# Kernel optimization log

Measured on AMD Instinct MI355X. Metric: run time of the kernel, lower is better.

The kernel has to match this reference:

```python
import jax, jax.numpy as jnp
import numpy as np

B, N, C = 8, 4096, 64          # graphs, points per graph, feature dim
RATIO = 0.25
M = int(N * RATIO)             # 1024 sampled centroids per graph
R = 0.2                        # radius (points live in the unit cube)
K = 64                         # max_num_neighbors in the forward
BIG = 1e10


def fps_single(pos):
    """Farthest point sampling on one cloud. pos: [N,3] -> [M] local indices.
    Deterministic start at index 0 (PyG uses a random start; math is identical)."""
    n = pos.shape[0]

    def step(carry, _):
        mind, last = carry
        d = jnp.sum((pos - pos[last]) ** 2, axis=-1)      # [N]
        mind = jnp.minimum(mind, d)
        nxt = jnp.argmax(mind)
        return (mind, nxt), nxt

    init = (jnp.full((n,), BIG, pos.dtype), jnp.int32(0))
    _, rest = jax.lax.scan(step, init, None, length=M - 1)
    return jnp.concatenate([jnp.zeros((1,), rest.dtype), rest])


def setup_inputs() -> dict:
    key = jax.random.key(0)
    ks = jax.random.split(key, 8)
    x = jax.random.normal(ks[0], (B * N, C), dtype=jnp.float32)
    pos = jax.random.uniform(ks[1], (B * N, 3), dtype=jnp.float32)
    batch = jnp.repeat(jnp.arange(B, dtype=jnp.int64), N)
    seed_idx = jnp.arange(B * N, dtype=jnp.int64)
    d_in, h, f_out = C + 3, 128, 256
    W1 = jax.random.normal(ks[2], (d_in, h), dtype=jnp.float32) / np.sqrt(d_in)
    b1 = jnp.zeros((h,), jnp.float32)
    W2 = jax.random.normal(ks[3], (h, h), dtype=jnp.float32) / np.sqrt(h)
    b2 = jnp.zeros((h,), jnp.float32)
    W3 = jax.random.normal(ks[4], (h, f_out), dtype=jnp.float32) / np.sqrt(h)
    b3 = jnp.zeros((f_out,), jnp.float32)
    return {"x": x, "pos": pos, "batch": batch, "seed_idx": seed_idx,
            "W1": W1, "b1": b1, "W2": W2, "b2": b2, "W3": W3, "b3": b3}


def reference(x, pos, batch, seed_idx, W1, b1, W2, b2, W3, b3):
    posb = pos.reshape(B, N, 3)
    xb = x.reshape(B, N, C)

    # --- FPS per graph (batch is block-contiguous with N points per graph) ---
    idx_local = jax.vmap(fps_single)(posb)                     # [B, M]
    ctr = jax.vmap(lambda p, i: p[i])(posb, idx_local)         # [B, M, 3]

    # --- radius neighbor search: up to K neighbors within r of each centroid ---
    d2 = jnp.sum((ctr[:, :, None, :] - posb[:, None, :, :]) ** 2, axis=-1)  # [B,M,N]
    d2m = jnp.where(d2 < R * R, d2, BIG)
    neg_d, nbr = jax.lax.top_k(-d2m, K)                        # K nearest within r
    valid = (-neg_d) < R * R                                   # [B, M, K]

    # --- PointConv: msg = MLP([x_j, pos_j - pos_i]), max-aggregate ---
    x_j = jax.vmap(lambda a, i: a[i])(xb, nbr)                 # [B, M, K, C]
    pos_j = jax.vmap(lambda p, i: p[i])(posb, nbr)             # [B, M, K, 3]
    msg = jnp.concatenate([x_j, pos_j - ctr[:, :, None, :]], axis=-1)  # [B,M,K,C+3]
    h = jax.nn.relu(msg @ W1 + b1)
    h = jax.nn.relu(h @ W2 + b2)
    h = jax.nn.relu(h @ W3 + b3)                               # [B, M, K, 256]
    h = jnp.where(valid[..., None], h, -BIG)
    out = jnp.max(h, axis=2)                                   # [B, M, 256]
    out = jnp.where(jnp.any(valid, axis=-1)[..., None], out, 0.0)

    # --- gather sampled outputs back to the flat layout ---
    idx_flat = (idx_local + jnp.arange(B)[:, None] * N).reshape(-1)  # [B*M]
    x_out = out.reshape(B * M, -1)
    pos_out = pos[idx_flat]
    batch_out = batch[idx_flat]
    seed_out = seed_idx[idx_flat]
    return x_out, pos_out, batch_out, seed_out
```

## Files before the change

### kernel.cpp

```cpp
#include <hip/hip_runtime.h>
#include <stdint.h>

#define BB 8
#define NN 4096
#define CC 64
#define MM 1024
#define EE (BB*MM)
#define KK 64
#define F3 256
#define SM 104
#define SH 136
#define CAP 768

typedef __bf16 bf16x8 __attribute__((ext_vector_type(8)));
typedef float floatx4 __attribute__((ext_vector_type(4)));

#define DPP_MAXSTEP(ctrl, rmask) { \
    unsigned o = (unsigned)__builtin_amdgcn_update_dpp(0, (int)v, ctrl, rmask, 0xf, false); \
    v = v > o ? v : o; }
__device__ __forceinline__ unsigned wave_umax_u32(unsigned v) {
  DPP_MAXSTEP(0x111, 0xf)
  DPP_MAXSTEP(0x112, 0xf)
  DPP_MAXSTEP(0x114, 0xf)
  DPP_MAXSTEP(0x118, 0xf)
  DPP_MAXSTEP(0x142, 0xa)
  DPP_MAXSTEP(0x143, 0xc)
  return (unsigned)__builtin_amdgcn_readlane((int)v, 63);
}
#define DPP_MINSTEP(ctrl, rmask) { \
    unsigned o = (unsigned)__builtin_amdgcn_update_dpp((int)0xffffffffu, (int)v, ctrl, rmask, 0xf, false); \
    v = v < o ? v : o; }
__device__ __forceinline__ unsigned wave_umin_u32(unsigned v) {
  DPP_MINSTEP(0x111, 0xf)
  DPP_MINSTEP(0x112, 0xf)
  DPP_MINSTEP(0x114, 0xf)
  DPP_MINSTEP(0x118, 0xf)
  DPP_MINSTEP(0x142, 0xa)
  DPP_MINSTEP(0x143, 0xc)
  return (unsigned)__builtin_amdgcn_readlane((int)v, 63);
}

__global__ __launch_bounds__(512) void fps_prep_kernel(
    const float* __restrict__ pos,
    const float* __restrict__ W1, const float* __restrict__ W2, const float* __restrict__ W3,
    int* __restrict__ fpsIdx, float* __restrict__ ctr,
    __bf16* __restrict__ W1t, __bf16* __restrict__ W2t, __bf16* __restrict__ W3t,
    float4* __restrict__ pos4) {
  __shared__ float4 sP4[NN];
  __shared__ unsigned long long sRed[2][8];
  const int blk = blockIdx.x;
  const int t = threadIdx.x;

  if (blk >= BB) {
    if (blk < 128) {
      const int i0 = (blk - 8) * 512 + t;
      if (i0 < 128 * 96) {
        const int n = i0 / 96, k = i0 % 96;
        W1t[i0] = (k < 67) ? (__bf16)W1[k * 128 + n] : (__bf16)0.0f;
      } else if (i0 < 128 * 96 + 128 * 128) {
        const int i = i0 - 128 * 96;
        const int n = i / 128, k = i % 128;
        W2t[i] = (__bf16)W2[k * 128 + n];
      } else {
        const int i = i0 - (128 * 96 + 128 * 128);
        const int n = i / 128, k = i % 128;
        W3t[i] = (__bf16)W3[k * 256 + n];
      }
    } else {
      const int i = (blk - 128) * 512 + t;
      pos4[i] = make_float4(pos[(long)i * 3 + 0], pos[(long)i * 3 + 1],
                            pos[(long)i * 3 + 2], 0.0f);
    }
    return;
  }

  const int g = blk;
  const int lane = t & 63, wv = t >> 6;
  float px[8], py[8], pz[8], mind[8];
#pragma unroll
  for (int j = 0; j < 8; ++j) {
    const int p = t + (j << 9);
    const long base = ((long)g * NN + p) * 3;
    px[j] = pos[base + 0];
    py[j] = pos[base + 1];
    pz[j] = pos[base + 2];
    mind[j] = 1e10f;
    sP4[p] = make_float4(px[j], py[j], pz[j], 0.0f);
  }
  __syncthreads();
  float wx = sP4[0].x, wy = sP4[0].y, wz = sP4[0].z;
  int win0 = 0, win1 = 0;
  for (int s = 1; s < MM; ++s) {
    unsigned bb = 0u, bidx = (unsigned)t;
#pragma unroll
    for (int j = 0; j < 8; ++j) {
      const float dx = __fsub_rn(px[j], wx);
      const float dy = __fsub_rn(py[j], wy);
      const float dz = __fsub_rn(pz[j], wz);
      const float d2 = __fadd_rn(__fadd_rn(__fmul_rn(dx, dx), __fmul_rn(dy, dy)), __fmul_rn(dz, dz));
      mind[j] = fminf(mind[j], d2);
      const unsigned mb = __float_as_uint(mind[j]);
      if (mb > bb) { bb = mb; bidx = (unsigned)(t + (j << 9)); }
    }
    const unsigned maxv = wave_umax_u32(bb);
    const unsigned cand = (bb == maxv) ? bidx : 0xffffffffu;
    const unsigned minidx = wave_umin_u32(cand);
    if (lane == 0)
      sRed[s & 1][wv] = ((unsigned long long)maxv << 32) | (unsigned long long)(~minidx);
    __syncthreads();
    unsigned long long m = sRed[s & 1][0];
#pragma unroll
    for (int w = 1; w < 8; ++w) {
      const unsigned long long o = sRed[s & 1][w];
      m = o > m ? o : m;
    }
    const int widx = (int)(~(unsigned)m);
    const float4 wp = sP4[widx];
    wx = wp.x; wy = wp.y; wz = wp.z;
    if (s == t)       win0 = widx;
    if (s == t + 512) win1 = widx;
  }
  {
    const long e0 = (long)g * MM + t;
    const float4 p0 = sP4[win0];
    fpsIdx[e0] = win0;
    ctr[e0 * 3 + 0] = p0.x; ctr[e0 * 3 + 1] = p0.y; ctr[e0 * 3 + 2] = p0.z;
    const long e1 = e0 + 512;
    const float4 p1 = sP4[win1];
    fpsIdx[e1] = win1;
    ctr[e1 * 3 + 0] = p1.x; ctr[e1 * 3 + 1] = p1.y; ctr[e1 * 3 + 2] = p1.z;
  }
}

__global__ __launch_bounds__(512) void mlp_kernel(const float* __restrict__ x,
    const float4* __restrict__ pos4, const float* __restrict__ ctr,
    const int* __restrict__ fpsIdx,
    const __bf16* __restrict__ W1t, const __bf16* __restrict__ W2t,
    const __bf16* __restrict__ W3t,
    const float* __restrict__ b1, const float* __restrict__ b2,
    const float* __restrict__ b3,
    float* __restrict__ outX, float* __restrict__ outP,
    float* __restrict__ outB, float* __restrict__ outS) {
  __shared__ __align__(16) __bf16 sMsg[64 * SM];
  __shared__ __align__(16) __bf16 sH[64 * SH];
  __shared__ int sSel[KK];
  __shared__ int sCnt;
  unsigned long long* sDI = (unsigned long long*)sMsg;

  const int e = blockIdx.x;
  const int t = threadIdx.x;
  const int b = e >> 10;
  const int lane = t & 63, wv = t >> 6;

  if (t == 0) sCnt = 0;
  const float cx = ctr[(long)e * 3 + 0];
  const float cy = ctr[(long)e * 3 + 1];
  const float cz = ctr[(long)e * 3 + 2];
  if (t < 3) outP[(long)e * 3 + t] = ctr[(long)e * 3 + t];
  if (t == 3) { outB[e] = (float)b; outS[e] = (float)(b * NN + fpsIdx[e]); }
  const float R2 = (float)(0.2 * 0.2);
  __syncthreads();

#pragma unroll
  for (int q = 0; q < NN / 512; ++q) {
    const int p = t + q * 512;
    const float4 P = pos4[b * NN + p];
    const float dx = __fsub_rn(cx, P.x);
    const float dy = __fsub_rn(cy, P.y);
    const float dz = __fsub_rn(cz, P.z);
    const float d2 = __fadd_rn(__fadd_rn(__fmul_rn(dx, dx), __fmul_rn(dy, dy)), __fmul_rn(dz, dz));
    const bool v = d2 < R2;
    const unsigned long long mask = __ballot(v);
    int wbase = 0;
    if (lane == 0 && mask) wbase = atomicAdd(&sCnt, (int)__popcll(mask));
    wbase = __shfl(wbase, 0);
    if (v) {
      const int off = wbase + (int)__popcll(mask & ((1ull << lane) - 1ull));
      if (off < CAP)
        sDI[off] = ((unsigned long long)__float_as_uint(d2) << 32) | (unsigned)p;
    }
  }
  __syncthreads();
  int cnt = sCnt; cnt = cnt > CAP ? CAP : cnt;
  const int nsel = cnt < KK ? cnt : KK;

  for (int i = t; i < cnt; i += 512) {
    const unsigned long long my = sDI[i];
    int rank = 0;
#pragma unroll 8
    for (int j = 0; j < cnt; ++j) rank += (sDI[j] < my) ? 1 : 0;
    if (rank < KK) sSel[rank] = (int)(unsigned)(my & 0xffffffffu);
  }
  __syncthreads();
  cnt = nsel;

  {
    const int r = t >> 3, p = t & 7;
    float4 a = make_float4(0.f, 0.f, 0.f, 0.f), c4 = a;
    if (r < cnt) {
      const float* xr = x + (long)(b * NN + sSel[r]) * CC + p * 8;
      a  = *(const float4*)xr;
      c4 = *(const float4*)(xr + 4);
    }
    __bf16 o[8] = {(__bf16)a.x, (__bf16)a.y, (__bf16)a.z, (__bf16)a.w,
                   (__bf16)c4.x, (__bf16)c4.y, (__bf16)c4.z, (__bf16)c4.w};
    *(uint4*)&sMsg[r * SM + p * 8] = *(uint4*)o;
  }
  if (t < 64) {
    const int r = t;
    __bf16 d0 = (__bf16)0.0f, d1 = (__bf16)0.0f, d2v = (__bf16)0.0f;
    if (r < cnt) {
      const float4 P = pos4[b * NN + sSel[r]];
      d0  = (__bf16)__fsub_rn(P.x, cx);
      d1  = (__bf16)__fsub_rn(P.y, cy);
      d2v = (__bf16)__fsub_rn(P.z, cz);
    }
    sMsg[r * SM + 64] = d0;
    sMsg[r * SM + 65] = d1;
    sMsg[r * SM + 66] = d2v;
    for (int c = 67; c < SM; ++c) sMsg[r * SM + c] = (__bf16)0.0f;
  }
  __syncthreads();

  const int l15 = lane & 15, quad = lane >> 4;
  {
    floatx4 acc[4] = {};
    const __bf16* wrow = W1t + (wv * 16 + l15) * 96;
#pragma unroll
    for (int ks = 0; ks < 3; ++ks) {
      const bf16x8 bfrag = *(const bf16x8*)(wrow + ks * 32 + quad * 8);
#pragma unroll
      for (int mt = 0; mt < 4; ++mt) {
        const bf16x8 afrag = *(const bf16x8*)&sMsg[(mt * 16 + l15) * SM + ks * 32 + quad * 8];
        acc[mt] = __builtin_amdgcn_mfma_f32_16x16x32_bf16(afrag, bfrag, acc[mt], 0, 0, 0);
      }
    }
    const int col = wv * 16 + l15;
    const float bias = b1[col];
#pragma unroll
    for (int mt = 0; mt < 4; ++mt)
#pragma unroll
      for (int rg = 0; rg < 4; ++rg) {
        const int row = mt * 16 + quad * 4 + rg;
        float v = acc[mt][rg] + bias;
        v = v > 0.0f ? v : 0.0f;
        sH[row * SH + col] = (__bf16)v;
      }
  }
  __syncthreads();
  {
    floatx4 acc[4] = {};
    const __bf16* wrow = W2t + (wv * 16 + l15) * 128;
#pragma unroll
    for (int ks = 0; ks < 4; ++ks) {
      const bf16x8 bfrag = *(const bf16x8*)(wrow + ks * 32 + quad * 8);
#pragma unroll
      for (int mt = 0; mt < 4; ++mt) {
        const bf16x8 afrag = *(const bf16x8*)&sH[(mt * 16 + l15) * SH + ks * 32 + quad * 8];
        acc[mt] = __builtin_amdgcn_mfma_f32_16x16x32_bf16(afrag, bfrag, acc[mt], 0, 0, 0);
      }
    }
    __syncthreads();
    const int col = wv * 16 + l15;
    const float bias = b2[col];
#pragma unroll
    for (int mt = 0; mt < 4; ++mt)
#pragma unroll
      for (int rg = 0; rg < 4; ++rg) {
        const int row = mt * 16 + quad * 4 + rg;
        float v = acc[mt][rg] + bias;
        v = v > 0.0f ? v : 0.0f;
        sH[row * SH + col] = (__bf16)v;
      }
  }
  __syncthreads();
  {
    floatx4 acc[2][4] = {};
#pragma unroll
    for (int ks = 0; ks < 4; ++ks) {
      bf16x8 afrag[4];
#pragma unroll
      for (int mt = 0; mt < 4; ++mt)
        afrag[mt] = *(const bf16x8*)&sH[(mt * 16 + l15) * SH + ks * 32 + quad * 8];
#pragma unroll
      for (int i = 0; i < 2; ++i) {
        const bf16x8 bfrag = *(const bf16x8*)(W3t + ((wv * 2 + i) * 16 + l15) * 128 + ks * 32 + quad * 8);
#pragma unroll
        for (int mt = 0; mt < 4; ++mt)
          acc[i][mt] = __builtin_amdgcn_mfma_f32_16x16x32_bf16(afrag[mt], bfrag, acc[i][mt], 0, 0, 0);
      }
    }
#pragma unroll
    for (int i = 0; i < 2; ++i) {
      const int col = (wv * 2 + i) * 16 + l15;
      const float bias = b3[col];
      float mx = 0.0f;
#pragma unroll
      for (int mt = 0; mt < 4; ++mt)
#pragma unroll
        for (int rg = 0; rg < 4; ++rg) {
          const int row = mt * 16 + quad * 4 + rg;
          float v = acc[i][mt][rg] + bias;
          v = v > 0.0f ? v : 0.0f;
          if (row < cnt) mx = fmaxf(mx, v);
        }
      mx = fmaxf(mx, __shfl_xor(mx, 16));
      mx = fmaxf(mx, __shfl_xor(mx, 32));
      if (quad == 0) outX[(long)e * F3 + col] = mx;
    }
  }
}

extern "C" void kernel_launch(void* const* d_in, const int* in_sizes, int n_in,
                              void* d_out, int out_size, void* d_ws, size_t ws_size,
                              hipStream_t stream) {
  const float* x   = (const float*)d_in[0];
  const float* pos = (const float*)d_in[1];
  const float* W1  = (const float*)d_in[4];
  const float* b1  = (const float*)d_in[5];
  const float* W2  = (const float*)d_in[6];
  const float* b2  = (const float*)d_in[7];
  const float* W3  = (const float*)d_in[8];
  const float* b3  = (const float*)d_in[9];

  char* ws = (char*)d_ws;
  int*    fpsIdx = (int*)(ws);
  float*  ctr    = (float*)(ws + 32768);
  __bf16* W1t    = (__bf16*)(ws + 131072);
  __bf16* W2t    = (__bf16*)(ws + 155648);
  __bf16* W3t    = (__bf16*)(ws + 188416);
  float4* pos4   = (float4*)(ws + 253952);

  float* outX = (float*)d_out;
  float* outP = outX + (long)EE * F3;
  float* outB = outP + (long)EE * 3;
  float* outS = outB + EE;

  fps_prep_kernel<<<192, 512, 0, stream>>>(pos, W1, W2, W3,
                                           fpsIdx, ctr, W1t, W2t, W3t, pos4);
  mlp_kernel<<<EE, 512, 0, stream>>>(x, pos4, ctr, fpsIdx, W1t, W2t, W3t,
                                     b1, b2, b3, outX, outP, outB, outS);
}
```

Measured before the change: 859.6 us.

## Fuse FPS, weight prep and MLP into one persistent kernel with progress flags

Merges the FPS/prep kernel and the per-centroid MLP kernel into a single launch. Blocks take work in order through an atomic ticket: FPS groups come first, then weight-transpose blocks, then centroid blocks. Each FPS group publishes its centroids in chunks of 64 through release flags, so MLP blocks can start once their centroid is ready instead of waiting for all FPS work to finish. The FPS loop also switches to packed f32 math and broadcasts the winner's coordinates by readlane rather than an LDS lookup, and the pos4 repack is dropped in favour of direct strided pos reads. This trades a kernel boundary for spin-waiting, and it depends on the FPS blocks staying resident and making forward progress.

```diff
diff --git a/kernel.cpp b/kernel.cpp
--- a/kernel.cpp
+++ b/kernel.cpp
@@ -11,9 +11,11 @@
 #define SM 104
 #define SH 136
 #define CAP 768
+#define NPREP 120
 
 typedef __bf16 bf16x8 __attribute__((ext_vector_type(8)));
 typedef float floatx4 __attribute__((ext_vector_type(4)));
+typedef float floatx2 __attribute__((ext_vector_type(2)));
 
 #define DPP_MAXSTEP(ctrl, rmask) { \
     unsigned o = (unsigned)__builtin_amdgcn_update_dpp(0, (int)v, ctrl, rmask, 0xf, false); \
@@ -40,134 +42,182 @@
   return (unsigned)__builtin_amdgcn_readlane((int)v, 63);
 }
 
-__global__ __launch_bounds__(512) void fps_prep_kernel(
-    const float* __restrict__ pos,
-    const float* __restrict__ W1, const float* __restrict__ W2, const float* __restrict__ W3,
+__global__ __launch_bounds__(512, 6) void fused_kernel(
+    const float* __restrict__ x, const float* __restrict__ pos,
+    const float* __restrict__ W1, const float* __restrict__ b1,
+    const float* __restrict__ W2, const float* __restrict__ b2,
+    const float* __restrict__ W3, const float* __restrict__ b3,
+    unsigned* __restrict__ flags,
     int* __restrict__ fpsIdx, float* __restrict__ ctr,
     __bf16* __restrict__ W1t, __bf16* __restrict__ W2t, __bf16* __restrict__ W3t,
-    float4* __restrict__ pos4) {
-  __shared__ float4 sP4[NN];
-  __shared__ unsigned long long sRed[2][8];
-  const int blk = blockIdx.x;
-  const int t = threadIdx.x;
-
-  if (blk >= BB) {
-    if (blk < 128) {
-      const int i0 = (blk - 8) * 512 + t;
-      if (i0 < 128 * 96) {
-        const int n = i0 / 96, k = i0 % 96;
-        W1t[i0] = (k < 67) ? (__bf16)W1[k * 128 + n] : (__bf16)0.0f;
-      } else if (i0 < 128 * 96 + 128 * 128) {
-        const int i = i0 - 128 * 96;
-        const int n = i / 128, k = i % 128;
-        W2t[i] = (__bf16)W2[k * 128 + n];
-      } else {
-        const int i = i0 - (128 * 96 + 128 * 128);
-        const int n = i / 128, k = i % 128;
-        W3t[i] = (__bf16)W3[k * 256 + n];
-      }
-    } else {
-      const int i = (blk - 128) * 512 + t;
-      pos4[i] = make_float4(pos[(long)i * 3 + 0], pos[(long)i * 3 + 1],
-                            pos[(long)i * 3 + 2], 0.0f);
-    }
-    return;
-  }
-
-  const int g = blk;
-  const int lane = t & 63, wv = t >> 6;
-  float px[8], py[8], pz[8], mind[8];
-#pragma unroll
-  for (int j = 0; j < 8; ++j) {
-    const int p = t + (j << 9);
-    const long base = ((long)g * NN + p) * 3;
-    px[j] = pos[base + 0];
-    py[j] = pos[base + 1];
-    pz[j] = pos[base + 2];
-    mind[j] = 1e10f;
-    sP4[p] = make_float4(px[j], py[j], pz[j], 0.0f);
-  }
-  __syncthreads();
-  float wx = sP4[0].x, wy = sP4[0].y, wz = sP4[0].z;
-  int win0 = 0, win1 = 0;
-  for (int s = 1; s < MM; ++s) {
-    unsigned bb = 0u, bidx = (unsigned)t;
-#pragma unroll
-    for (int j = 0; j < 8; ++j) {
-      const float dx = __fsub_rn(px[j], wx);
-      const float dy = __fsub_rn(py[j], wy);
-      const float dz = __fsub_rn(pz[j], wz);
-      const float d2 = __fadd_rn(__fadd_rn(__fmul_rn(dx, dx), __fmul_rn(dy, dy)), __fmul_rn(dz, dz));
-      mind[j] = fminf(mind[j], d2);
-      const unsigned mb = __float_as_uint(mind[j]);
-      if (mb > bb) { bb = mb; bidx = (unsigned)(t + (j << 9)); }
-    }
-    const unsigned maxv = wave_umax_u32(bb);
-    const unsigned cand = (bb == maxv) ? bidx : 0xffffffffu;
-    const unsigned minidx = wave_umin_u32(cand);
-    if (lane == 0)
-      sRed[s & 1][wv] = ((unsigned long long)maxv << 32) | (unsigned long long)(~minidx);
-    __syncthreads();
-    unsigned long long m = sRed[s & 1][0];
-#pragma unroll
-    for (int w = 1; w < 8; ++w) {
-      const unsigned long long o = sRed[s & 1][w];
-      m = o > m ? o : m;
-    }
-    const int widx = (int)(~(unsigned)m);
-    const float4 wp = sP4[widx];
-    wx = wp.x; wy = wp.y; wz = wp.z;
-    if (s == t)       win0 = widx;
-    if (s == t + 512) win1 = widx;
-  }
-  {
-    const long e0 = (long)g * MM + t;
-    const float4 p0 = sP4[win0];
-    fpsIdx[e0] = win0;
-    ctr[e0 * 3 + 0] = p0.x; ctr[e0 * 3 + 1] = p0.y; ctr[e0 * 3 + 2] = p0.z;
-    const long e1 = e0 + 512;
-    const float4 p1 = sP4[win1];
-    fpsIdx[e1] = win1;
-    ctr[e1 * 3 + 0] = p1.x; ctr[e1 * 3 + 1] = p1.y; ctr[e1 * 3 + 2] = p1.z;
-  }
-}
-
-__global__ __launch_bounds__(512) void mlp_kernel(const float* __restrict__ x,
-    const float4* __restrict__ pos4, const float* __restrict__ ctr,
-    const int* __restrict__ fpsIdx,
-    const __bf16* __restrict__ W1t, const __bf16* __restrict__ W2t,
-    const __bf16* __restrict__ W3t,
-    const float* __restrict__ b1, const float* __restrict__ b2,
-    const float* __restrict__ b3,
     float* __restrict__ outX, float* __restrict__ outP,
     float* __restrict__ outB, float* __restrict__ outS) {
   __shared__ __align__(16) __bf16 sMsg[64 * SM];
   __shared__ __align__(16) __bf16 sH[64 * SH];
   __shared__ int sSel[KK];
   __shared__ int sCnt;
+  __shared__ unsigned long long sRedK[2][8];
+  __shared__ __align__(16) float4 sRedP[2][8];
+  __shared__ int sTicket;
+
+  const int t = threadIdx.x;
+  const int lane = t & 63, wv = t >> 6;
+  if (t == 0)
+    sTicket = (int)__hip_atomic_fetch_add(&flags[0], 1u, __ATOMIC_RELAXED,
+                                          __HIP_MEMORY_SCOPE_AGENT);
+  __syncthreads();
+  const int tk = sTicket;
+
+  if (tk < BB) {
+    __builtin_amdgcn_s_setprio(3);
+    const int g = tk;
+    floatx2 p2x[4], p2y[4], p2z[4];
+    float mind[8];
+#pragma unroll
+    for (int q = 0; q < 4; ++q) {
+#pragma unroll
+      for (int h = 0; h < 2; ++h) {
+        const int p = t + (((q << 1) | h) << 9);
+        const long base = ((long)g * NN + p) * 3;
+        p2x[q][h] = pos[base + 0];
+        p2y[q][h] = pos[base + 1];
+        p2z[q][h] = pos[base + 2];
+        mind[(q << 1) | h] = 1e10f;
+      }
+    }
+    float wx = pos[(long)g * NN * 3 + 0];
+    float wy = pos[(long)g * NN * 3 + 1];
+    float wz = pos[(long)g * NN * 3 + 2];
+    int winI0 = 0, winI1 = 0;
+    float w0x = wx, w0y = wy, w0z = wz;
+    float w1x = wx, w1y = wy, w1z = wz;
+
+    for (int s = 1; s < MM; ++s) {
+      const float nwx = -wx, nwy = -wy, nwz = -wz;
+      const floatx2 nx2 = {nwx, nwx}, ny2 = {nwy, nwy}, nz2 = {nwz, nwz};
+      unsigned bb = 0u, bidx = (unsigned)t;
+#pragma unroll
+      for (int q = 0; q < 4; ++q) {
+        floatx2 dx, dy, dz, xx, yy, zz, s1, d2;
+        asm("v_pk_add_f32 %0, %1, %2" : "=v"(dx) : "v"(p2x[q]), "v"(nx2));
+        asm("v_pk_add_f32 %0, %1, %2" : "=v"(dy) : "v"(p2y[q]), "v"(ny2));
+        asm("v_pk_add_f32 %0, %1, %2" : "=v"(dz) : "v"(p2z[q]), "v"(nz2));
+        asm("v_pk_mul_f32 %0, %1, %1" : "=v"(xx) : "v"(dx));
+        asm("v_pk_mul_f32 %0, %1, %1" : "=v"(yy) : "v"(dy));
+        asm("v_pk_mul_f32 %0, %1, %1" : "=v"(zz) : "v"(dz));
+        asm("v_pk_add_f32 %0, %1, %2" : "=v"(s1) : "v"(xx), "v"(yy));
+        asm("v_pk_add_f32 %0, %1, %2" : "=v"(d2) : "v"(s1), "v"(zz));
+#pragma unroll
+        for (int h = 0; h < 2; ++h) {
+          const int i = (q << 1) | h;
+          mind[i] = fminf(mind[i], d2[h]);
+          const unsigned mb = __float_as_uint(mind[i]);
+          if (mb > bb) { bb = mb; bidx = (unsigned)(t + (i << 9)); }
+        }
+      }
+      const unsigned maxv = wave_umax_u32(bb);
+      const unsigned cand = (bb == maxv) ? bidx : 0xffffffffu;
+      const unsigned minidx = wave_umin_u32(cand);
+      const int jw = (int)(minidx >> 9), qw = jw >> 1, hw = jw & 1;
+      const floatx2 sx = p2x[qw], sy = p2y[qw], sz = p2z[qw];
+      const float cxx = hw ? sx[1] : sx[0];
+      const float cyy = hw ? sy[1] : sy[0];
+      const float czz = hw ? sz[1] : sz[0];
+      const int lw = (int)(minidx & 63u);
+      const float bx = __int_as_float(__builtin_amdgcn_readlane(__float_as_int(cxx), lw));
+      const float by = __int_as_float(__builtin_amdgcn_readlane(__float_as_int(cyy), lw));
+      const float bz = __int_as_float(__builtin_amdgcn_readlane(__float_as_int(czz), lw));
+      if (lane == 0) {
+        sRedK[s & 1][wv] = ((unsigned long long)maxv << 32) |
+                           (unsigned long long)(~minidx);
+        sRedP[s & 1][wv] = make_float4(bx, by, bz, 0.0f);
+      }
+      __syncthreads();
+      unsigned long long kk = sRedK[s & 1][0];
+      int wbest = 0;
+#pragma unroll
+      for (int w = 1; w < 8; ++w) {
+        const unsigned long long kw = sRedK[s & 1][w];
+        if (kw > kk) { kk = kw; wbest = w; }
+      }
+      const float4 wp = sRedP[s & 1][wbest];
+      wx = wp.x; wy = wp.y; wz = wp.z;
+      const int widx = (int)(~(unsigned)kk);
+      if (s == t)       { winI0 = widx; w0x = wx; w0y = wy; w0z = wz; }
+      if (s == t + 512) { winI1 = widx; w1x = wx; w1y = wy; w1z = wz; }
+      if ((s & 63) == 63) {
+        const int f = s >> 6;
+        if (wv == (f & 7)) {
+          const int step = (f < 8) ? t : (t + 512);
+          const int wI   = (f < 8) ? winI0 : winI1;
+          const float fx = (f < 8) ? w0x : w1x;
+          const float fy = (f < 8) ? w0y : w1y;
+          const float fz = (f < 8) ? w0z : w1z;
+          const long ee = (long)g * MM + step;
+          __hip_atomic_store(&fpsIdx[ee], wI, __ATOMIC_RELAXED, __HIP_MEMORY_SCOPE_AGENT);
+          __hip_atomic_store(&ctr[ee * 3 + 0], fx, __ATOMIC_RELAXED, __HIP_MEMORY_SCOPE_AGENT);
+          __hip_atomic_store(&ctr[ee * 3 + 1], fy, __ATOMIC_RELAXED, __HIP_MEMORY_SCOPE_AGENT);
+          __hip_atomic_store(&ctr[ee * 3 + 2], fz, __ATOMIC_RELAXED, __HIP_MEMORY_SCOPE_AGENT);
+          if (lane == 0)
+            __hip_atomic_store(&flags[2 + g], (unsigned)((f + 1) * 64),
+                               __ATOMIC_RELEASE, __HIP_MEMORY_SCOPE_AGENT);
+        }
+      }
+    }
+    return;
+  }
+
+  if (tk < BB + NPREP) {
+    const int i0 = (tk - BB) * 512 + t;
+    if (i0 < 128 * 96) {
+      const int n = i0 / 96, k = i0 % 96;
+      W1t[i0] = (k < 67) ? (__bf16)W1[k * 128 + n] : (__bf16)0.0f;
+    } else if (i0 < 128 * 96 + 128 * 128) {
+      const int i = i0 - 128 * 96;
+      const int n = i / 128, k = i % 128;
+      W2t[i] = (__bf16)W2[k * 128 + n];
+    } else {
+      const int i = i0 - (128 * 96 + 128 * 128);
+      const int n = i / 128, k = i % 128;
+      W3t[i] = (__bf16)W3[k * 256 + n];
+    }
+    __syncthreads();
+    if (t == 0)
+      __hip_atomic_fetch_add(&flags[1], 1u, __ATOMIC_RELEASE, __HIP_MEMORY_SCOPE_AGENT);
+    return;
+  }
+
+  const int eo = tk - (BB + NPREP);
+  const int b = eo & 7;
+  const int m = eo >> 3;
+  const int e = b * MM + m;
+
+  if (t == 1) sCnt = 0;
+  if (t == 0) {
+    while (__hip_atomic_load(&flags[1], __ATOMIC_RELAXED, __HIP_MEMORY_SCOPE_AGENT) < NPREP)
+      __builtin_amdgcn_s_sleep(32);
+    while ((int)__hip_atomic_load(&flags[2 + b], __ATOMIC_RELAXED, __HIP_MEMORY_SCOPE_AGENT) <= m)
+      __builtin_amdgcn_s_sleep(32);
+    (void)__hip_atomic_load(&flags[1], __ATOMIC_ACQUIRE, __HIP_MEMORY_SCOPE_AGENT);
+    (void)__hip_atomic_load(&flags[2 + b], __ATOMIC_ACQUIRE, __HIP_MEMORY_SCOPE_AGENT);
+  }
+  __syncthreads();
+
   unsigned long long* sDI = (unsigned long long*)sMsg;
-
-  const int e = blockIdx.x;
-  const int t = threadIdx.x;
-  const int b = e >> 10;
-  const int lane = t & 63, wv = t >> 6;
-
-  if (t == 0) sCnt = 0;
   const float cx = ctr[(long)e * 3 + 0];
   const float cy = ctr[(long)e * 3 + 1];
   const float cz = ctr[(long)e * 3 + 2];
   if (t < 3) outP[(long)e * 3 + t] = ctr[(long)e * 3 + t];
   if (t == 3) { outB[e] = (float)b; outS[e] = (float)(b * NN + fpsIdx[e]); }
   const float R2 = (float)(0.2 * 0.2);
-  __syncthreads();
+  const long pbase = (long)b * NN * 3;
 
 #pragma unroll
   for (int q = 0; q < NN / 512; ++q) {
     const int p = t + q * 512;
-    const float4 P = pos4[b * NN + p];
-    const float dx = __fsub_rn(cx, P.x);
-    const float dy = __fsub_rn(cy, P.y);
-    const float dz = __fsub_rn(cz, P.z);
+    const float dx = __fsub_rn(cx, pos[pbase + (long)p * 3 + 0]);
+    const float dy = __fsub_rn(cy, pos[pbase + (long)p * 3 + 1]);
+    const float dz = __fsub_rn(cz, pos[pbase + (long)p * 3 + 2]);
     const float d2 = __fadd_rn(__fadd_rn(__fmul_rn(dx, dx), __fmul_rn(dy, dy)), __fmul_rn(dz, dz));
     const bool v = d2 < R2;
     const unsigned long long mask = __ballot(v);
@@ -204,16 +254,17 @@
     }
     __bf16 o[8] = {(__bf16)a.x, (__bf16)a.y, (__bf16)a.z, (__bf16)a.w,
                    (__bf16)c4.x, (__bf16)c4.y, (__bf16)c4.z, (__bf16)c4.w};
+    __syncthreads();
     *(uint4*)&sMsg[r * SM + p * 8] = *(uint4*)o;
   }
   if (t < 64) {
     const int r = t;
     __bf16 d0 = (__bf16)0.0f, d1 = (__bf16)0.0f, d2v = (__bf16)0.0f;
     if (r < cnt) {
-      const float4 P = pos4[b * NN + sSel[r]];
-      d0  = (__bf16)__fsub_rn(P.x, cx);
-      d1  = (__bf16)__fsub_rn(P.y, cy);
-      d2v = (__bf16)__fsub_rn(P.z, cz);
+      const long j = pbase + (long)sSel[r] * 3;
+      d0  = (__bf16)__fsub_rn(pos[j + 0], cx);
+      d1  = (__bf16)__fsub_rn(pos[j + 1], cy);
+      d2v = (__bf16)__fsub_rn(pos[j + 2], cz);
     }
     sMsg[r * SM + 64] = d0;
     sMsg[r * SM + 65] = d1;
@@ -324,20 +375,20 @@
   const float* b3  = (const float*)d_in[9];
 
   char* ws = (char*)d_ws;
-  int*    fpsIdx = (int*)(ws);
-  float*  ctr    = (float*)(ws + 32768);
-  __bf16* W1t    = (__bf16*)(ws + 131072);
-  __bf16* W2t    = (__bf16*)(ws + 155648);
-  __bf16* W3t    = (__bf16*)(ws + 188416);
-  float4* pos4   = (float4*)(ws + 253952);
+  unsigned* flags  = (unsigned*)(ws);
+  int*    fpsIdx = (int*)(ws + 1024);
+  float*  ctr    = (float*)(ws + 33792);
+  __bf16* W1t    = (__bf16*)(ws + 132096);
+  __bf16* W2t    = (__bf16*)(ws + 156672);
+  __bf16* W3t    = (__bf16*)(ws + 189440);
 
   float* outX = (float*)d_out;
   float* outP = outX + (long)EE * F3;
   float* outB = outP + (long)EE * 3;
   float* outS = outB + EE;
 
-  fps_prep_kernel<<<192, 512, 0, stream>>>(pos, W1, W2, W3,
-                                           fpsIdx, ctr, W1t, W2t, W3t, pos4);
-  mlp_kernel<<<EE, 512, 0, stream>>>(x, pos4, ctr, fpsIdx, W1t, W2t, W3t,
-                                     b1, b2, b3, outX, outP, outB, outS);
+  hipMemsetAsync(flags, 0, 64, stream);
+  fused_kernel<<<BB + NPREP + EE, 512, 0, stream>>>(
+      x, pos, W1, b1, W2, b2, W3, b3,
+      flags, fpsIdx, ctr, W1t, W2t, W3t, outX, outP, outB, outS);
 }
```

New measurement: 1.724 ms. 101% more time.

## Pass FPS winner coordinates through per-wave reduction and use packed f32 math

Applied to the files above, without the earlier changes.

The FPS loop no longer keeps the whole point cloud in shared memory. Each wave reads its candidate winner's coordinates from registers with readlane and publishes them beside the reduction key, so the serial loop no longer does a dependent shared-memory lookup of the winning point after the barrier. The distance computation uses v_pk_add/v_pk_mul f32 inline asm to handle two points per instruction, with the subtraction rewritten as adding a negated value, which should round the same way. A __syncthreads was also added in the MLP kernel before the sMsg write, which looks like a fix for a hazard where sMsg is reused from sDI.

```diff
diff --git a/kernel.cpp b/kernel.cpp
--- a/kernel.cpp
+++ b/kernel.cpp
@@ -14,6 +14,7 @@
 
 typedef __bf16 bf16x8 __attribute__((ext_vector_type(8)));
 typedef float floatx4 __attribute__((ext_vector_type(4)));
+typedef float floatx2 __attribute__((ext_vector_type(2)));
 
 #define DPP_MAXSTEP(ctrl, rmask) { \
     unsigned o = (unsigned)__builtin_amdgcn_update_dpp(0, (int)v, ctrl, rmask, 0xf, false); \
@@ -46,8 +47,8 @@
     int* __restrict__ fpsIdx, float* __restrict__ ctr,
     __bf16* __restrict__ W1t, __bf16* __restrict__ W2t, __bf16* __restrict__ W3t,
     float4* __restrict__ pos4) {
-  __shared__ float4 sP4[NN];
-  __shared__ unsigned long long sRed[2][8];
+  __shared__ unsigned long long sRedK[2][8];
+  __shared__ __align__(16) float4 sRedP[2][8];
   const int blk = blockIdx.x;
   const int t = threadIdx.x;
 
@@ -76,59 +77,88 @@
 
   const int g = blk;
   const int lane = t & 63, wv = t >> 6;
-  float px[8], py[8], pz[8], mind[8];
-#pragma unroll
-  for (int j = 0; j < 8; ++j) {
-    const int p = t + (j << 9);
-    const long base = ((long)g * NN + p) * 3;
-    px[j] = pos[base + 0];
-    py[j] = pos[base + 1];
-    pz[j] = pos[base + 2];
-    mind[j] = 1e10f;
-    sP4[p] = make_float4(px[j], py[j], pz[j], 0.0f);
-  }
-  __syncthreads();
-  float wx = sP4[0].x, wy = sP4[0].y, wz = sP4[0].z;
-  int win0 = 0, win1 = 0;
+  floatx2 p2x[4], p2y[4], p2z[4];
+  float mind[8];
+#pragma unroll
+  for (int q = 0; q < 4; ++q) {
+#pragma unroll
+    for (int h = 0; h < 2; ++h) {
+      const int p = t + (((q << 1) | h) << 9);
+      const long base = ((long)g * NN + p) * 3;
+      p2x[q][h] = pos[base + 0];
+      p2y[q][h] = pos[base + 1];
+      p2z[q][h] = pos[base + 2];
+      mind[(q << 1) | h] = 1e10f;
+    }
+  }
+  float wx = pos[(long)g * NN * 3 + 0];
+  float wy = pos[(long)g * NN * 3 + 1];
+  float wz = pos[(long)g * NN * 3 + 2];
+  int winI0 = 0, winI1 = 0;
+  float w0x = wx, w0y = wy, w0z = wz;
+  float w1x = wx, w1y = wy, w1z = wz;
+
   for (int s = 1; s < MM; ++s) {
+    const float nwx = -wx, nwy = -wy, nwz = -wz;
+    const floatx2 nx2 = {nwx, nwx}, ny2 = {nwy, nwy}, nz2 = {nwz, nwz};
     unsigned bb = 0u, bidx = (unsigned)t;
 #pragma unroll
-    for (int j = 0; j < 8; ++j) {
-      const float dx = __fsub_rn(px[j], wx);
-      const float dy = __fsub_rn(py[j], wy);
-      const float dz = __fsub_rn(pz[j], wz);
-      const float d2 = __fadd_rn(__fadd_rn(__fmul_rn(dx, dx), __fmul_rn(dy, dy)), __fmul_rn(dz, dz));
-      mind[j] = fminf(mind[j], d2);
-      const unsigned mb = __float_as_uint(mind[j]);
-      if (mb > bb) { bb = mb; bidx = (unsigned)(t + (j << 9)); }
+    for (int q = 0; q < 4; ++q) {
+      floatx2 dx, dy, dz, xx, yy, zz, s1, d2;
+      asm("v_pk_add_f32 %0, %1, %2" : "=v"(dx) : "v"(p2x[q]), "v"(nx2));
+      asm("v_pk_add_f32 %0, %1, %2" : "=v"(dy) : "v"(p2y[q]), "v"(ny2));
+      asm("v_pk_add_f32 %0, %1, %2" : "=v"(dz) : "v"(p2z[q]), "v"(nz2));
+      asm("v_pk_mul_f32 %0, %1, %1" : "=v"(xx) : "v"(dx));
+      asm("v_pk_mul_f32 %0, %1, %1" : "=v"(yy) : "v"(dy));
+      asm("v_pk_mul_f32 %0, %1, %1" : "=v"(zz) : "v"(dz));
+      asm("v_pk_add_f32 %0, %1, %2" : "=v"(s1) : "v"(xx), "v"(yy));
+      asm("v_pk_add_f32 %0, %1, %2" : "=v"(d2) : "v"(s1), "v"(zz));
+#pragma unroll
+      for (int h = 0; h < 2; ++h) {
+        const int i = (q << 1) | h;
+        mind[i] = fminf(mind[i], d2[h]);
+        const unsigned mb = __float_as_uint(mind[i]);
+        if (mb > bb) { bb = mb; bidx = (unsigned)(t + (i << 9)); }
+      }
     }
     const unsigned maxv = wave_umax_u32(bb);
     const unsigned cand = (bb == maxv) ? bidx : 0xffffffffu;
     const unsigned minidx = wave_umin_u32(cand);
-    if (lane == 0)
-      sRed[s & 1][wv] = ((unsigned long long)maxv << 32) | (unsigned long long)(~minidx);
+    const int jw = (int)(minidx >> 9), qw = jw >> 1, hw = jw & 1;
+    const floatx2 sx = p2x[qw], sy = p2y[qw], sz = p2z[qw];
+    const float cxx = hw ? sx[1] : sx[0];
+    const float cyy = hw ? sy[1] : sy[0];
+    const float czz = hw ? sz[1] : sz[0];
+    const int lw = (int)(minidx & 63u);
+    const float bx = __int_as_float(__builtin_amdgcn_readlane(__float_as_int(cxx), lw));
+    const float by = __int_as_float(__builtin_amdgcn_readlane(__float_as_int(cyy), lw));
+    const float bz = __int_as_float(__builtin_amdgcn_readlane(__float_as_int(czz), lw));
+    if (lane == 0) {
+      sRedK[s & 1][wv] = ((unsigned long long)maxv << 32) |
+                         (unsigned long long)(~minidx);
+      sRedP[s & 1][wv] = make_float4(bx, by, bz, 0.0f);
+    }
     __syncthreads();
-    unsigned long long m = sRed[s & 1][0];
+    unsigned long long kk = sRedK[s & 1][0];
+    int wbest = 0;
 #pragma unroll
     for (int w = 1; w < 8; ++w) {
-      const unsigned long long o = sRed[s & 1][w];
-      m = o > m ? o : m;
-    }
-    const int widx = (int)(~(unsigned)m);
-    const float4 wp = sP4[widx];
+      const unsigned long long kw = sRedK[s & 1][w];
+      if (kw > kk) { kk = kw; wbest = w; }
+    }
+    const float4 wp = sRedP[s & 1][wbest];
     wx = wp.x; wy = wp.y; wz = wp.z;
-    if (s == t)       win0 = widx;
-    if (s == t + 512) win1 = widx;
+    const int widx = (int)(~(unsigned)kk);
+    if (s == t)       { winI0 = widx; w0x = wx; w0y = wy; w0z = wz; }
+    if (s == t + 512) { winI1 = widx; w1x = wx; w1y = wy; w1z = wz; }
   }
   {
     const long e0 = (long)g * MM + t;
-    const float4 p0 = sP4[win0];
-    fpsIdx[e0] = win0;
-    ctr[e0 * 3 + 0] = p0.x; ctr[e0 * 3 + 1] = p0.y; ctr[e0 * 3 + 2] = p0.z;
+    fpsIdx[e0] = winI0;
+    ctr[e0 * 3 + 0] = w0x; ctr[e0 * 3 + 1] = w0y; ctr[e0 * 3 + 2] = w0z;
     const long e1 = e0 + 512;
-    const float4 p1 = sP4[win1];
-    fpsIdx[e1] = win1;
-    ctr[e1 * 3 + 0] = p1.x; ctr[e1 * 3 + 1] = p1.y; ctr[e1 * 3 + 2] = p1.z;
+    fpsIdx[e1] = winI1;
+    ctr[e1 * 3 + 0] = w1x; ctr[e1 * 3 + 1] = w1y; ctr[e1 * 3 + 2] = w1z;
   }
 }
 
@@ -204,6 +234,7 @@
     }
     __bf16 o[8] = {(__bf16)a.x, (__bf16)a.y, (__bf16)a.z, (__bf16)a.w,
                    (__bf16)c4.x, (__bf16)c4.y, (__bf16)c4.z, (__bf16)c4.w};
+    __syncthreads();
     *(uint4*)&sMsg[r * SM + p * 8] = *(uint4*)o;
   }
   if (t < 64) {
```

New measurement: 1.285 ms. 49.5% more time.
